# Optimization experiments

Measured on AMD Instinct MI355X. Metric: run time of the kernel, lower is better.

The kernel has to match this reference:

```python
import jax, jax.numpy as jnp
import numpy as np

DT_NS = 8.0
ALPHA, BETA, GAMMA, RISE_W = 0.7, 0.2, 0.1, 0.05
DECAY_TAUS = jnp.array([40.0, 300.0, 230.0, 2.4], dtype=jnp.float32)
RISE_TAUS = jnp.array([5.0, 20.0, 10.0, 2.0], dtype=jnp.float32)
TAIL = 195  # tail window: [peak+5, peak+200)


def setup_inputs() -> dict:
    key = jax.random.key(0)
    k1, k2, k3, k4 = jax.random.split(key, 4)
    B, S, C = 32768, 1024, 4
    return {
        "logits": jax.random.normal(k1, (B, C), dtype=jnp.float32),
        "labels": jax.random.randint(k2, (B,), 0, C, dtype=jnp.int64),
        "waveforms": jax.random.uniform(k3, (B, S), dtype=jnp.float32),
        "amplitudes": jax.random.uniform(k4, (B,), dtype=jnp.float32),
    }


def _masked_mean(vals, valid):
    w = valid.astype(vals.dtype)
    n = jnp.sum(w)
    return jnp.where(n > 0, jnp.sum(vals * w) / jnp.maximum(n, 1.0), 0.0)


def _decay_time_loss(waveforms, pred_cls):
    B, S = waveforms.shape
    peak = jnp.argmax(waveforms, axis=1)                      # (B,)
    valid = peak < S - 20
    # fixed-size tail window starting at peak+5, masked past end of record
    idx = peak[:, None] + 5 + jnp.arange(TAIL)[None, :]       # (B, TAIL)
    in_range = idx < S
    tail = jnp.take_along_axis(waveforms, jnp.minimum(idx, S - 1), axis=1)
    pos = in_range & (tail > 0)                               # positive-sample mask
    w = pos.astype(jnp.float32)
    n_pos = jnp.sum(w, axis=1)
    valid &= n_pos >= 5
    t = (jnp.arange(TAIL, dtype=jnp.float32) * DT_NS)[None, :]
    log_tail = jnp.log(jnp.where(pos, tail, 1.0) + 1e-8)
    n_safe = jnp.maximum(n_pos, 1.0)
    t_mean = jnp.sum(w * t, axis=1) / n_safe
    y_mean = jnp.sum(w * log_tail, axis=1) / n_safe
    dt_c = t - t_mean[:, None]
    num = jnp.sum(w * dt_c * (log_tail - y_mean[:, None]), axis=1)
    den = jnp.sum(w * dt_c * dt_c, axis=1)
    valid &= den > 0
    slope = num / jnp.maximum(den, 1e-30)
    fitted_tau = -1.0 / (slope + 1e-8)
    tau_loss = (fitted_tau - DECAY_TAUS[pred_cls]) ** 2
    return _masked_mean(tau_loss, valid)


def _energy_conservation_loss(waveforms, amplitudes):
    charge = jnp.sum(jnp.maximum(waveforms, 0.0), axis=1)
    ratio = charge / (amplitudes + 1e-8)
    return jnp.var(ratio, ddof=1)  # torch.var default is unbiased


def _rise_time_loss(waveforms, pred_cls):
    B, S = waveforms.shape
    peak = jnp.argmax(waveforms, axis=1)
    amp = jnp.take_along_axis(waveforms, peak[:, None], axis=1)[:, 0]
    valid = peak >= 10
    edge = jnp.arange(S)[None, :] < peak[:, None]             # rising edge mask
    ab10 = edge & (waveforms >= 0.1 * amp[:, None])
    ab90 = edge & (waveforms >= 0.9 * amp[:, None])
    valid &= jnp.any(ab10, axis=1) & jnp.any(ab90, axis=1)
    idx10 = jnp.argmax(ab10, axis=1).astype(jnp.float32)      # first crossing
    idx90 = jnp.argmax(ab90, axis=1).astype(jnp.float32)
    rise = (idx90 - idx10) * DT_NS
    exp_rise = RISE_TAUS[pred_cls]
    rt_loss = jnp.abs(rise - exp_rise) / exp_rise
    return _masked_mean(rt_loss, valid)


def reference(logits, labels, waveforms, amplitudes):
    logp = jax.nn.log_softmax(logits, axis=-1)
    ce = -jnp.mean(jnp.take_along_axis(logp, labels[:, None], axis=1)[:, 0])
    pred_cls = jnp.argmax(logits, axis=1)
    decay = _decay_time_loss(waveforms, pred_cls)
    energy = _energy_conservation_loss(waveforms, amplitudes)
    rise = _rise_time_loss(waveforms, pred_cls)
    total = ALPHA * ce + BETA * decay + GAMMA * energy + RISE_W * rise
    return total, ce, decay, energy, rise
```

## Files before the change

### kernel.cpp

```cpp
#include <hip/hip_runtime.h>
#include <cmath>

#define BROWS 32768
#define SLEN  1024
#define TAILW 195
#define NB1   2048
#define NB2   128

__device__ __constant__ float c_decay_taus[4] = {40.0f, 300.0f, 230.0f, 2.4f};
__device__ __constant__ float c_rise_taus[4]  = {5.0f, 20.0f, 10.0f, 2.0f};

struct alignas(16) RowStat {
    unsigned nSk;
    unsigned Skk;
    float    csum;
    unsigned pki;
    double   Sy;
    double   Sky;
};

extern "C" __global__ __launch_bounds__(256, 8)
void physics_rows(const float* __restrict__ wave, RowStat* __restrict__ stats)
{
    const int lane  = threadIdx.x & 63;
    const int wid   = threadIdx.x >> 6;
    const int gwave = blockIdx.x * 4 + wid;
    const int nwaves = NB1 * 4;
    const int lane4 = lane * 4;
    const float4* base = reinterpret_cast<const float4*>(wave);

    int row = gwave;
    const float4* p0 = base + (size_t)row * (SLEN / 4) + lane;
    float4 c0 = p0[0], c1 = p0[64], c2 = p0[128], c3 = p0[192];

    #pragma unroll
    for (int it = 0; it < 4; ++it) {
        const int nrow = row + nwaves;
        float4 n0, n1, n2, n3;
        if (it < 3) {
            const float4* pn = base + (size_t)nrow * (SLEN / 4) + lane;
            n0 = pn[0]; n1 = pn[64]; n2 = pn[128]; n3 = pn[192];
        }

        float vals[16] = {c0.x,c0.y,c0.z,c0.w, c1.x,c1.y,c1.z,c1.w,
                          c2.x,c2.y,c2.z,c2.w, c3.x,c3.y,c3.z,c3.w};

        float m0 = fmaxf(fmaxf(vals[0],  vals[1]),  vals[2]);
        float m1 = fmaxf(fmaxf(vals[3],  vals[4]),  vals[5]);
        float m2 = fmaxf(fmaxf(vals[6],  vals[7]),  vals[8]);
        float m3 = fmaxf(fmaxf(vals[9],  vals[10]), vals[11]);
        float m4 = fmaxf(fmaxf(vals[12], vals[13]), fmaxf(vals[14], vals[15]));
        float bm = fmaxf(fmaxf(fmaxf(m0, m1), m2), fmaxf(m3, m4));

        float s0 = 0.f, s1 = 0.f, s2 = 0.f, s3 = 0.f;
        #pragma unroll
        for (int k = 0; k < 16; k += 4) {
            s0 += fmaxf(vals[k],     0.0f);
            s1 += fmaxf(vals[k + 1], 0.0f);
            s2 += fmaxf(vals[k + 2], 0.0f);
            s3 += fmaxf(vals[k + 3], 0.0f);
        }
        float csum = (s0 + s1) + (s2 + s3);

        #pragma unroll
        for (int off = 1; off < 64; off <<= 1) {
            bm   = fmaxf(bm, __shfl_xor(bm, off, 64));
            csum += __shfl_xor(csum, off, 64);
        }
        const float amp = bm;

        int peak = SLEN;
        #pragma unroll
        for (int q = 0; q < 4; ++q) {
            bool found = false;
            #pragma unroll
            for (int r = 0; r < 4; ++r) {
                const unsigned long long b = __ballot(vals[q * 4 + r] == amp);
                if (b) {
                    peak = min(peak, q * 256 + 4 * (__ffsll(b) - 1) + r);
                    found = true;
                }
            }
            if (found) break;
        }
        peak = __builtin_amdgcn_readfirstlane(peak);
        const bool do_decay = (peak < SLEN - 20);
        const int  pm5 = peak + 5;

        const float t10 = 0.1f * amp, t90 = 0.9f * amp;
        int i10 = SLEN, i90 = SLEN;
        #pragma unroll
        for (int q = 0; q < 4; ++q) {
            #pragma unroll
            for (int r = 0; r < 4; ++r) {
                const int jb = q * 256 + r;
                const int d  = peak - jb;
                if (d > 0) {
                    const int lc = min(64, (d + 3) >> 2);
                    const unsigned long long lm =
                        (lc >= 64) ? ~0ull : ((1ull << lc) - 1ull);
                    const float w = vals[q * 4 + r];
                    const unsigned long long b10 = __ballot(w >= t10) & lm;
                    const unsigned long long b90 = __ballot(w >= t90) & lm;
                    if (b10) i10 = min(i10, jb + 4 * (__ffsll(b10) - 1));
                    if (b90) i90 = min(i90, jb + 4 * (__ffsll(b90) - 1));
                }
            }
        }

        unsigned nSk_p = 0, Skk = 0;
        double Sy = 0.0, Sky = 0.0;
        if (do_decay) {
            #pragma unroll
            for (int q = 0; q < 4; ++q) {
                if (q * 256 + 255 >= pm5 && q * 256 <= pm5 + (TAILW - 1)) {
                    #pragma unroll
                    for (int r = 0; r < 4; ++r) {
                        const int kk = q * 256 + lane4 + r - pm5;
                        const float w = vals[q * 4 + r];
                        if ((unsigned)kk < (unsigned)TAILW && w > 0.0f) {
                            const float y = __logf(w + 1e-8f);
                            nSk_p += 1u + ((unsigned)kk << 8);
                            Skk   += (unsigned)(kk * kk);
                            Sy  += (double)y;
                            Sky += (double)kk * (double)y;
                        }
                    }
                }
            }
        }

        #pragma unroll
        for (int off = 1; off < 64; off <<= 1) {
            nSk_p += __shfl_xor(nSk_p, off, 64);
            Skk   += __shfl_xor(Skk,   off, 64);
            Sy    += __shfl_xor(Sy,    off, 64);
            Sky   += __shfl_xor(Sky,   off, 64);
        }

        if (lane == 0) {
            RowStat st;
            st.nSk  = (nSk_p & 0xFFu) | ((nSk_p >> 8) << 16);
            st.Skk  = Skk;
            st.csum = csum;
            st.pki  = ((unsigned)peak << 22) | ((unsigned)i10 << 11) | (unsigned)i90;
            st.Sy   = Sy;
            st.Sky  = Sky;
            stats[row] = st;
        }

        if (it < 3) { c0 = n0; c1 = n1; c2 = n2; c3 = n3; row = nrow; }
    }
}

extern "C" __global__ __launch_bounds__(256)
void physics_rowfin(const RowStat* __restrict__ stats,
                    const float* __restrict__ logits,
                    const int* __restrict__ labels,
                    const float* __restrict__ amps,
                    double* __restrict__ partials)
{
    const int r    = blockIdx.x * 256 + threadIdx.x;
    const int lane = threadIdx.x & 63;
    const int wid  = threadIdx.x >> 6;

    const RowStat st = stats[r];
    const unsigned n_u  = st.nSk & 0xFFFFu;
    const unsigned Sk_u = st.nSk >> 16;
    const int peak = (int)(st.pki >> 22);
    const int i10  = (int)((st.pki >> 11) & 0x7FFu);
    const int i90  = (int)(st.pki & 0x7FFu);

    const float4 l4 = reinterpret_cast<const float4*>(logits)[r];
    float lg[4] = {l4.x, l4.y, l4.z, l4.w};
    int pred = 0; float pbest = lg[0];
    #pragma unroll
    for (int c = 1; c < 4; ++c) if (lg[c] > pbest) { pbest = lg[c]; pred = c; }
    const float m = fmaxf(fmaxf(lg[0], lg[1]), fmaxf(lg[2], lg[3]));
    const float sexp = expf(lg[0] - m) + expf(lg[1] - m)
                     + expf(lg[2] - m) + expf(lg[3] - m);
    const float lse = m + logf(sexp);
    const double v0 = (double)(lse - lg[labels[r]]);

    double v1 = 0.0, v2 = 0.0;
    if (peak < SLEN - 20 && n_u >= 5u) {
        const double dn  = (double)n_u;
        const double dSk = (double)Sk_u;
        const double num = st.Sky - dSk * st.Sy / dn;
        const double den = 8.0 * ((double)st.Skk - dSk * dSk / dn);
        if (den > 0.0) {
            const double slope = num / fmax(den, 1e-30);
            const double tau   = -1.0 / (slope + 1e-8);
            const double d     = tau - (double)c_decay_taus[pred];
            v1 = d * d; v2 = 1.0;
        }
    }
    double v3 = 0.0, v4 = 0.0;
    if (peak >= 10 && i10 < SLEN && i90 < SLEN) {
        const float rise = (float)(i90 - i10) * 8.0f;
        const float er   = c_rise_taus[pred];
        v3 = (double)(fabsf(rise - er) / er); v4 = 1.0;
    }
    const double ratio = (double)st.csum / ((double)amps[r] + 1e-8);

    double v[7] = {v0, v1, v2, v3, v4, ratio, ratio * ratio};
    #pragma unroll
    for (int i = 0; i < 7; ++i) {
        #pragma unroll
        for (int off = 1; off < 64; off <<= 1)
            v[i] += __shfl_xor(v[i], off, 64);
    }
    __shared__ double sm[4][7];
    if (lane == 0) {
        #pragma unroll
        for (int i = 0; i < 7; ++i) sm[wid][i] = v[i];
    }
    __syncthreads();
    if (threadIdx.x < 7) {
        const int i = threadIdx.x;
        partials[(size_t)blockIdx.x * 7 + i] = sm[0][i] + sm[1][i] + sm[2][i] + sm[3][i];
    }
}

extern "C" __global__ void physics_finalize(const double* __restrict__ partials,
                                            float* __restrict__ out)
{
    const int t = threadIdx.x;
    double loc[7];
    #pragma unroll
    for (int i = 0; i < 7; ++i)
        loc[i] = partials[(size_t)t * 7 + i] + partials[(size_t)(t + 64) * 7 + i];
    #pragma unroll
    for (int i = 0; i < 7; ++i) {
        #pragma unroll
        for (int off = 1; off < 64; off <<= 1)
            loc[i] += __shfl_xor(loc[i], off, 64);
    }
    if (t == 0) {
        const double Bn = (double)BROWS;
        const double ce    = loc[0] / Bn;
        const double decay = (loc[2] > 0.0) ? loc[1] / fmax(loc[2], 1.0) : 0.0;
        const double rise  = (loc[4] > 0.0) ? loc[3] / fmax(loc[4], 1.0) : 0.0;
        const double var   = (loc[6] - loc[5] * loc[5] / Bn) / (Bn - 1.0);
        const double total = 0.7 * ce + 0.2 * decay + 0.1 * var + 0.05 * rise;
        out[0] = (float)total; out[1] = (float)ce; out[2] = (float)decay;
        out[3] = (float)var;   out[4] = (float)rise;
    }
}

extern "C" void kernel_launch(void* const* d_in, const int* in_sizes, int n_in,
                              void* d_out, int out_size, void* d_ws, size_t ws_size,
                              hipStream_t stream) {
    const float* logits = (const float*)d_in[0];
    const int*   labels = (const int*)d_in[1];
    const float* wave   = (const float*)d_in[2];
    const float* amps   = (const float*)d_in[3];

    RowStat* stats    = (RowStat*)d_ws;
    double*  partials = (double*)((char*)d_ws + (size_t)BROWS * sizeof(RowStat));

    physics_rows<<<NB1, 256, 0, stream>>>(wave, stats);
    physics_rowfin<<<NB2, 256, 0, stream>>>(stats, logits, labels, amps, partials);
    physics_finalize<<<1, 64, 0, stream>>>(partials, (float*)d_out);
}
```

Baseline: 46.13 us.

## Fuse row stats, per-row finalize and global reduction into one kernel

Merges the three kernels into a single kernel. Per-row statistics stay in shared memory and are finalized in-block rather than written to a workspace and re-read. A global atomic counter lets the last block reduce the per-block partials and write the outputs. This removes two kernel launches and the stats round trip through memory. In exchange it adds a memset, atomics and a serial tail in one block.

```diff
diff --git a/kernel.cpp b/kernel.cpp
--- a/kernel.cpp
+++ b/kernel.cpp
@@ -5,39 +5,42 @@
 #define SLEN  1024
 #define TAILW 195
 #define NB1   2048
-#define NB2   128
+#define NWAVES (NB1 * 4)
+#define RPW   4
+#define PART_STRIDE 2048
 
 __device__ __constant__ float c_decay_taus[4] = {40.0f, 300.0f, 230.0f, 2.4f};
 __device__ __constant__ float c_rise_taus[4]  = {5.0f, 20.0f, 10.0f, 2.0f};
 
-struct alignas(16) RowStat {
-    unsigned nSk;
-    unsigned Skk;
-    float    csum;
-    unsigned pki;
-    double   Sy;
-    double   Sky;
-};
-
 extern "C" __global__ __launch_bounds__(256, 8)
-void physics_rows(const float* __restrict__ wave, RowStat* __restrict__ stats)
+void physics_fused(const float* __restrict__ wave,
+                   const float* __restrict__ logits,
+                   const int*   __restrict__ labels,
+                   const float* __restrict__ amps,
+                   double* __restrict__ partials,
+                   unsigned* __restrict__ counter,
+                   float* __restrict__ out)
 {
     const int lane  = threadIdx.x & 63;
     const int wid   = threadIdx.x >> 6;
     const int gwave = blockIdx.x * 4 + wid;
-    const int nwaves = NB1 * 4;
     const int lane4 = lane * 4;
     const float4* base = reinterpret_cast<const float4*>(wave);
+
+    __shared__ unsigned su[4][RPW][4];
+    __shared__ double   sd[4][RPW][2];
+    __shared__ double   smp[4][7];
+    __shared__ int      s_last;
 
     int row = gwave;
     const float4* p0 = base + (size_t)row * (SLEN / 4) + lane;
     float4 c0 = p0[0], c1 = p0[64], c2 = p0[128], c3 = p0[192];
 
     #pragma unroll
-    for (int it = 0; it < 4; ++it) {
-        const int nrow = row + nwaves;
+    for (int it = 0; it < RPW; ++it) {
+        const int nrow = row + NWAVES;
         float4 n0, n1, n2, n3;
-        if (it < 3) {
+        if (it < RPW - 1) {
             const float4* pn = base + (size_t)nrow * (SLEN / 4) + lane;
             n0 = pn[0]; n1 = pn[64]; n2 = pn[128]; n3 = pn[192];
         }
@@ -139,109 +142,123 @@
         }
 
         if (lane == 0) {
-            RowStat st;
-            st.nSk  = (nSk_p & 0xFFu) | ((nSk_p >> 8) << 16);
-            st.Skk  = Skk;
-            st.csum = csum;
-            st.pki  = ((unsigned)peak << 22) | ((unsigned)i10 << 11) | (unsigned)i90;
-            st.Sy   = Sy;
-            st.Sky  = Sky;
-            stats[row] = st;
-        }
-
-        if (it < 3) { c0 = n0; c1 = n1; c2 = n2; c3 = n3; row = nrow; }
-    }
-}
-
-extern "C" __global__ __launch_bounds__(256)
-void physics_rowfin(const RowStat* __restrict__ stats,
-                    const float* __restrict__ logits,
-                    const int* __restrict__ labels,
-                    const float* __restrict__ amps,
-                    double* __restrict__ partials)
-{
-    const int r    = blockIdx.x * 256 + threadIdx.x;
-    const int lane = threadIdx.x & 63;
-    const int wid  = threadIdx.x >> 6;
-
-    const RowStat st = stats[r];
-    const unsigned n_u  = st.nSk & 0xFFFFu;
-    const unsigned Sk_u = st.nSk >> 16;
-    const int peak = (int)(st.pki >> 22);
-    const int i10  = (int)((st.pki >> 11) & 0x7FFu);
-    const int i90  = (int)(st.pki & 0x7FFu);
-
-    const float4 l4 = reinterpret_cast<const float4*>(logits)[r];
-    float lg[4] = {l4.x, l4.y, l4.z, l4.w};
-    int pred = 0; float pbest = lg[0];
-    #pragma unroll
-    for (int c = 1; c < 4; ++c) if (lg[c] > pbest) { pbest = lg[c]; pred = c; }
-    const float m = fmaxf(fmaxf(lg[0], lg[1]), fmaxf(lg[2], lg[3]));
-    const float sexp = expf(lg[0] - m) + expf(lg[1] - m)
-                     + expf(lg[2] - m) + expf(lg[3] - m);
-    const float lse = m + logf(sexp);
-    const double v0 = (double)(lse - lg[labels[r]]);
-
-    double v1 = 0.0, v2 = 0.0;
-    if (peak < SLEN - 20 && n_u >= 5u) {
-        const double dn  = (double)n_u;
-        const double dSk = (double)Sk_u;
-        const double num = st.Sky - dSk * st.Sy / dn;
-        const double den = 8.0 * ((double)st.Skk - dSk * dSk / dn);
-        if (den > 0.0) {
-            const double slope = num / fmax(den, 1e-30);
-            const double tau   = -1.0 / (slope + 1e-8);
-            const double d     = tau - (double)c_decay_taus[pred];
-            v1 = d * d; v2 = 1.0;
-        }
-    }
-    double v3 = 0.0, v4 = 0.0;
-    if (peak >= 10 && i10 < SLEN && i90 < SLEN) {
-        const float rise = (float)(i90 - i10) * 8.0f;
-        const float er   = c_rise_taus[pred];
-        v3 = (double)(fabsf(rise - er) / er); v4 = 1.0;
-    }
-    const double ratio = (double)st.csum / ((double)amps[r] + 1e-8);
-
-    double v[7] = {v0, v1, v2, v3, v4, ratio, ratio * ratio};
-    #pragma unroll
-    for (int i = 0; i < 7; ++i) {
-        #pragma unroll
-        for (int off = 1; off < 64; off <<= 1)
-            v[i] += __shfl_xor(v[i], off, 64);
-    }
-    __shared__ double sm[4][7];
+            su[wid][it][0] = nSk_p;
+            su[wid][it][1] = Skk;
+            su[wid][it][2] = __float_as_uint(csum);
+            su[wid][it][3] = ((unsigned)peak << 22) | ((unsigned)i10 << 11) | (unsigned)i90;
+            sd[wid][it][0] = Sy;
+            sd[wid][it][1] = Sky;
+        }
+
+        if (it < RPW - 1) { c0 = n0; c1 = n1; c2 = n2; c3 = n3; row = nrow; }
+    }
+
+    double v0 = 0, v1 = 0, v2 = 0, v3 = 0, v4 = 0, v5 = 0, v6 = 0;
+    if (lane < RPW) {
+        const int r = gwave + lane * NWAVES;
+        const unsigned nSk = su[wid][lane][0];
+        const unsigned Skk = su[wid][lane][1];
+        const float   csum = __uint_as_float(su[wid][lane][2]);
+        const unsigned pki = su[wid][lane][3];
+        const double  Sy   = sd[wid][lane][0];
+        const double  Sky  = sd[wid][lane][1];
+        const unsigned n_u  = nSk & 0xFFu;
+        const unsigned Sk_u = nSk >> 8;
+        const int peak = (int)(pki >> 22);
+        const int i10  = (int)((pki >> 11) & 0x7FFu);
+        const int i90  = (int)(pki & 0x7FFu);
+
+        const float4 l4 = reinterpret_cast<const float4*>(logits)[r];
+        float lg[4] = {l4.x, l4.y, l4.z, l4.w};
+        int pred = 0; float pbest = lg[0];
+        #pragma unroll
+        for (int c = 1; c < 4; ++c) if (lg[c] > pbest) { pbest = lg[c]; pred = c; }
+        const float m = fmaxf(fmaxf(lg[0], lg[1]), fmaxf(lg[2], lg[3]));
+        const float sexp = expf(lg[0] - m) + expf(lg[1] - m)
+                         + expf(lg[2] - m) + expf(lg[3] - m);
+        const float lse = m + logf(sexp);
+        v0 = (double)(lse - lg[labels[r]]);
+
+        if (peak < SLEN - 20 && n_u >= 5u) {
+            const double dn  = (double)n_u;
+            const double dSk = (double)Sk_u;
+            const double num = Sky - dSk * Sy / dn;
+            const double den = 8.0 * ((double)Skk - dSk * dSk / dn);
+            if (den > 0.0) {
+                const double slope = num / fmax(den, 1e-30);
+                const double tau   = -1.0 / (slope + 1e-8);
+                const double d     = tau - (double)c_decay_taus[pred];
+                v1 = d * d; v2 = 1.0;
+            }
+        }
+        if (peak >= 10 && i10 < SLEN && i90 < SLEN) {
+            const float rise = (float)(i90 - i10) * 8.0f;
+            const float er   = c_rise_taus[pred];
+            v3 = (double)(fabsf(rise - er) / er); v4 = 1.0;
+        }
+        v5 = (double)csum / ((double)amps[r] + 1e-8);
+        v6 = v5 * v5;
+    }
+    #pragma unroll
+    for (int off = 1; off <= 2; off <<= 1) {
+        v0 += __shfl_xor(v0, off, 64);
+        v1 += __shfl_xor(v1, off, 64);
+        v2 += __shfl_xor(v2, off, 64);
+        v3 += __shfl_xor(v3, off, 64);
+        v4 += __shfl_xor(v4, off, 64);
+        v5 += __shfl_xor(v5, off, 64);
+        v6 += __shfl_xor(v6, off, 64);
+    }
     if (lane == 0) {
-        #pragma unroll
-        for (int i = 0; i < 7; ++i) sm[wid][i] = v[i];
+        smp[wid][0] = v0; smp[wid][1] = v1; smp[wid][2] = v2; smp[wid][3] = v3;
+        smp[wid][4] = v4; smp[wid][5] = v5; smp[wid][6] = v6;
     }
     __syncthreads();
     if (threadIdx.x < 7) {
         const int i = threadIdx.x;
-        partials[(size_t)blockIdx.x * 7 + i] = sm[0][i] + sm[1][i] + sm[2][i] + sm[3][i];
-    }
-}
-
-extern "C" __global__ void physics_finalize(const double* __restrict__ partials,
-                                            float* __restrict__ out)
-{
-    const int t = threadIdx.x;
-    double loc[7];
-    #pragma unroll
-    for (int i = 0; i < 7; ++i)
-        loc[i] = partials[(size_t)t * 7 + i] + partials[(size_t)(t + 64) * 7 + i];
+        const double t = smp[0][i] + smp[1][i] + smp[2][i] + smp[3][i];
+        __hip_atomic_store(&partials[(size_t)i * PART_STRIDE + blockIdx.x], t,
+                           __ATOMIC_RELAXED, __HIP_MEMORY_SCOPE_AGENT);
+    }
+    __syncthreads();
+    if (threadIdx.x == 0) {
+        const unsigned prev = __hip_atomic_fetch_add(counter, 1u,
+                                  __ATOMIC_ACQ_REL, __HIP_MEMORY_SCOPE_AGENT);
+        s_last = (prev == NB1 - 1) ? 1 : 0;
+    }
+    __syncthreads();
+    if (!s_last) return;
+
+    double loc[7] = {0, 0, 0, 0, 0, 0, 0};
+    #pragma unroll
+    for (int k = 0; k < NB1 / 256; ++k) {
+        const int b = k * 256 + threadIdx.x;
+        #pragma unroll
+        for (int i = 0; i < 7; ++i)
+            loc[i] += __hip_atomic_load(&partials[(size_t)i * PART_STRIDE + b],
+                                        __ATOMIC_RELAXED, __HIP_MEMORY_SCOPE_AGENT);
+    }
     #pragma unroll
     for (int i = 0; i < 7; ++i) {
         #pragma unroll
         for (int off = 1; off < 64; off <<= 1)
             loc[i] += __shfl_xor(loc[i], off, 64);
     }
-    if (t == 0) {
+    if (lane == 0) {
+        #pragma unroll
+        for (int i = 0; i < 7; ++i) smp[wid][i] = loc[i];
+    }
+    __syncthreads();
+    if (threadIdx.x == 0) {
+        double t[7];
+        #pragma unroll
+        for (int i = 0; i < 7; ++i)
+            t[i] = smp[0][i] + smp[1][i] + smp[2][i] + smp[3][i];
         const double Bn = (double)BROWS;
-        const double ce    = loc[0] / Bn;
-        const double decay = (loc[2] > 0.0) ? loc[1] / fmax(loc[2], 1.0) : 0.0;
-        const double rise  = (loc[4] > 0.0) ? loc[3] / fmax(loc[4], 1.0) : 0.0;
-        const double var   = (loc[6] - loc[5] * loc[5] / Bn) / (Bn - 1.0);
+        const double ce    = t[0] / Bn;
+        const double decay = (t[2] > 0.0) ? t[1] / fmax(t[2], 1.0) : 0.0;
+        const double rise  = (t[4] > 0.0) ? t[3] / fmax(t[4], 1.0) : 0.0;
+        const double var   = (t[6] - t[5] * t[5] / Bn) / (Bn - 1.0);
         const double total = 0.7 * ce + 0.2 * decay + 0.1 * var + 0.05 * rise;
         out[0] = (float)total; out[1] = (float)ce; out[2] = (float)decay;
         out[3] = (float)var;   out[4] = (float)rise;
@@ -256,10 +273,10 @@
     const float* wave   = (const float*)d_in[2];
     const float* amps   = (const float*)d_in[3];
 
-    RowStat* stats    = (RowStat*)d_ws;
-    double*  partials = (double*)((char*)d_ws + (size_t)BROWS * sizeof(RowStat));
-
-    physics_rows<<<NB1, 256, 0, stream>>>(wave, stats);
-    physics_rowfin<<<NB2, 256, 0, stream>>>(stats, logits, labels, amps, partials);
-    physics_finalize<<<1, 64, 0, stream>>>(partials, (float*)d_out);
+    double*   partials = (double*)d_ws;
+    unsigned* counter  = (unsigned*)((char*)d_ws + 7 * PART_STRIDE * sizeof(double));
+
+    hipMemsetAsync(counter, 0, sizeof(unsigned), stream);
+    physics_fused<<<NB1, 256, 0, stream>>>(wave, logits, labels, amps,
+                                           partials, counter, (float*)d_out);
 }
```

After: 77.89 us. 1.69x slower.

## Drop software row pipelining and fold finalize into last-block reduction

Applied to the files above, without the earlier changes.

The row kernel now launches one wavefront per row (8192 blocks) instead of a persistent grid that prefetched the next row, so latency hiding relies on occupancy rather than explicit double-buffering. The separate finalize kernel is removed: each rowfin block publishes its partials, increments an atomic counter, and the last block performs the final reduction and writes outputs. This removes a kernel launch but adds a memset node and atomic synchronization.

```diff
diff --git a/kernel.cpp b/kernel.cpp
--- a/kernel.cpp
+++ b/kernel.cpp
@@ -4,8 +4,9 @@
 #define BROWS 32768
 #define SLEN  1024
 #define TAILW 195
-#define NB1   2048
+#define NB1   8192
 #define NB2   128
+#define PSTRIDE 128
 
 __device__ __constant__ float c_decay_taus[4] = {40.0f, 300.0f, 230.0f, 2.4f};
 __device__ __constant__ float c_rise_taus[4]  = {5.0f, 20.0f, 10.0f, 2.0f};
@@ -22,134 +23,117 @@
 extern "C" __global__ __launch_bounds__(256, 8)
 void physics_rows(const float* __restrict__ wave, RowStat* __restrict__ stats)
 {
-    const int lane  = threadIdx.x & 63;
-    const int wid   = threadIdx.x >> 6;
-    const int gwave = blockIdx.x * 4 + wid;
-    const int nwaves = NB1 * 4;
+    const int lane = threadIdx.x & 63;
+    const int row  = (blockIdx.x * 256 + threadIdx.x) >> 6;
     const int lane4 = lane * 4;
-    const float4* base = reinterpret_cast<const float4*>(wave);
-
-    int row = gwave;
-    const float4* p0 = base + (size_t)row * (SLEN / 4) + lane;
-    float4 c0 = p0[0], c1 = p0[64], c2 = p0[128], c3 = p0[192];
-
-    #pragma unroll
-    for (int it = 0; it < 4; ++it) {
-        const int nrow = row + nwaves;
-        float4 n0, n1, n2, n3;
-        if (it < 3) {
-            const float4* pn = base + (size_t)nrow * (SLEN / 4) + lane;
-            n0 = pn[0]; n1 = pn[64]; n2 = pn[128]; n3 = pn[192];
-        }
-
-        float vals[16] = {c0.x,c0.y,c0.z,c0.w, c1.x,c1.y,c1.z,c1.w,
-                          c2.x,c2.y,c2.z,c2.w, c3.x,c3.y,c3.z,c3.w};
-
-        float m0 = fmaxf(fmaxf(vals[0],  vals[1]),  vals[2]);
-        float m1 = fmaxf(fmaxf(vals[3],  vals[4]),  vals[5]);
-        float m2 = fmaxf(fmaxf(vals[6],  vals[7]),  vals[8]);
-        float m3 = fmaxf(fmaxf(vals[9],  vals[10]), vals[11]);
-        float m4 = fmaxf(fmaxf(vals[12], vals[13]), fmaxf(vals[14], vals[15]));
-        float bm = fmaxf(fmaxf(fmaxf(m0, m1), m2), fmaxf(m3, m4));
-
-        float s0 = 0.f, s1 = 0.f, s2 = 0.f, s3 = 0.f;
-        #pragma unroll
-        for (int k = 0; k < 16; k += 4) {
-            s0 += fmaxf(vals[k],     0.0f);
-            s1 += fmaxf(vals[k + 1], 0.0f);
-            s2 += fmaxf(vals[k + 2], 0.0f);
-            s3 += fmaxf(vals[k + 3], 0.0f);
-        }
-        float csum = (s0 + s1) + (s2 + s3);
-
-        #pragma unroll
-        for (int off = 1; off < 64; off <<= 1) {
-            bm   = fmaxf(bm, __shfl_xor(bm, off, 64));
-            csum += __shfl_xor(csum, off, 64);
-        }
-        const float amp = bm;
-
-        int peak = SLEN;
+    const float4* p = reinterpret_cast<const float4*>(wave) + (size_t)row * (SLEN / 4) + lane;
+
+    const float4 c0 = p[0], c1 = p[64], c2 = p[128], c3 = p[192];
+    float vals[16] = {c0.x,c0.y,c0.z,c0.w, c1.x,c1.y,c1.z,c1.w,
+                      c2.x,c2.y,c2.z,c2.w, c3.x,c3.y,c3.z,c3.w};
+
+    float m0 = fmaxf(fmaxf(vals[0],  vals[1]),  vals[2]);
+    float m1 = fmaxf(fmaxf(vals[3],  vals[4]),  vals[5]);
+    float m2 = fmaxf(fmaxf(vals[6],  vals[7]),  vals[8]);
+    float m3 = fmaxf(fmaxf(vals[9],  vals[10]), vals[11]);
+    float m4 = fmaxf(fmaxf(vals[12], vals[13]), fmaxf(vals[14], vals[15]));
+    float bm = fmaxf(fmaxf(fmaxf(m0, m1), m2), fmaxf(m3, m4));
+
+    float s0 = 0.f, s1 = 0.f, s2 = 0.f, s3 = 0.f;
+    #pragma unroll
+    for (int k = 0; k < 16; k += 4) {
+        s0 += fmaxf(vals[k],     0.0f);
+        s1 += fmaxf(vals[k + 1], 0.0f);
+        s2 += fmaxf(vals[k + 2], 0.0f);
+        s3 += fmaxf(vals[k + 3], 0.0f);
+    }
+    float csum = (s0 + s1) + (s2 + s3);
+
+    #pragma unroll
+    for (int off = 1; off < 64; off <<= 1) {
+        bm   = fmaxf(bm, __shfl_xor(bm, off, 64));
+        csum += __shfl_xor(csum, off, 64);
+    }
+    const float amp = bm;
+
+    int peak = SLEN;
+    #pragma unroll
+    for (int q = 0; q < 4; ++q) {
+        bool found = false;
+        #pragma unroll
+        for (int r = 0; r < 4; ++r) {
+            const unsigned long long b = __ballot(vals[q * 4 + r] == amp);
+            if (b) {
+                peak = min(peak, q * 256 + 4 * (__ffsll(b) - 1) + r);
+                found = true;
+            }
+        }
+        if (found) break;
+    }
+    peak = __builtin_amdgcn_readfirstlane(peak);
+    const bool do_decay = (peak < SLEN - 20);
+    const int  pm5 = peak + 5;
+
+    const float t10 = 0.1f * amp, t90 = 0.9f * amp;
+    int i10 = SLEN, i90 = SLEN;
+    #pragma unroll
+    for (int q = 0; q < 4; ++q) {
+        #pragma unroll
+        for (int r = 0; r < 4; ++r) {
+            const int jb = q * 256 + r;
+            const int d  = peak - jb;
+            if (d > 0) {
+                const int lc = min(64, (d + 3) >> 2);
+                const unsigned long long lm =
+                    (lc >= 64) ? ~0ull : ((1ull << lc) - 1ull);
+                const float w = vals[q * 4 + r];
+                const unsigned long long b10 = __ballot(w >= t10) & lm;
+                const unsigned long long b90 = __ballot(w >= t90) & lm;
+                if (b10) i10 = min(i10, jb + 4 * (__ffsll(b10) - 1));
+                if (b90) i90 = min(i90, jb + 4 * (__ffsll(b90) - 1));
+            }
+        }
+    }
+
+    unsigned nSk_p = 0, Skk = 0;
+    double Sy = 0.0, Sky = 0.0;
+    if (do_decay) {
         #pragma unroll
         for (int q = 0; q < 4; ++q) {
-            bool found = false;
-            #pragma unroll
-            for (int r = 0; r < 4; ++r) {
-                const unsigned long long b = __ballot(vals[q * 4 + r] == amp);
-                if (b) {
-                    peak = min(peak, q * 256 + 4 * (__ffsll(b) - 1) + r);
-                    found = true;
-                }
-            }
-            if (found) break;
-        }
-        peak = __builtin_amdgcn_readfirstlane(peak);
-        const bool do_decay = (peak < SLEN - 20);
-        const int  pm5 = peak + 5;
-
-        const float t10 = 0.1f * amp, t90 = 0.9f * amp;
-        int i10 = SLEN, i90 = SLEN;
-        #pragma unroll
-        for (int q = 0; q < 4; ++q) {
-            #pragma unroll
-            for (int r = 0; r < 4; ++r) {
-                const int jb = q * 256 + r;
-                const int d  = peak - jb;
-                if (d > 0) {
-                    const int lc = min(64, (d + 3) >> 2);
-                    const unsigned long long lm =
-                        (lc >= 64) ? ~0ull : ((1ull << lc) - 1ull);
+            if (q * 256 + 255 >= pm5 && q * 256 <= pm5 + (TAILW - 1)) {
+                #pragma unroll
+                for (int r = 0; r < 4; ++r) {
+                    const int kk = q * 256 + lane4 + r - pm5;
                     const float w = vals[q * 4 + r];
-                    const unsigned long long b10 = __ballot(w >= t10) & lm;
-                    const unsigned long long b90 = __ballot(w >= t90) & lm;
-                    if (b10) i10 = min(i10, jb + 4 * (__ffsll(b10) - 1));
-                    if (b90) i90 = min(i90, jb + 4 * (__ffsll(b90) - 1));
-                }
-            }
-        }
-
-        unsigned nSk_p = 0, Skk = 0;
-        double Sy = 0.0, Sky = 0.0;
-        if (do_decay) {
-            #pragma unroll
-            for (int q = 0; q < 4; ++q) {
-                if (q * 256 + 255 >= pm5 && q * 256 <= pm5 + (TAILW - 1)) {
-                    #pragma unroll
-                    for (int r = 0; r < 4; ++r) {
-                        const int kk = q * 256 + lane4 + r - pm5;
-                        const float w = vals[q * 4 + r];
-                        if ((unsigned)kk < (unsigned)TAILW && w > 0.0f) {
-                            const float y = __logf(w + 1e-8f);
-                            nSk_p += 1u + ((unsigned)kk << 8);
-                            Skk   += (unsigned)(kk * kk);
-                            Sy  += (double)y;
-                            Sky += (double)kk * (double)y;
-                        }
+                    if ((unsigned)kk < (unsigned)TAILW && w > 0.0f) {
+                        const float y = __logf(w + 1e-8f);
+                        nSk_p += 1u + ((unsigned)kk << 8);
+                        Skk   += (unsigned)(kk * kk);
+                        Sy  += (double)y;
+                        Sky += (double)kk * (double)y;
                     }
                 }
             }
         }
-
-        #pragma unroll
-        for (int off = 1; off < 64; off <<= 1) {
-            nSk_p += __shfl_xor(nSk_p, off, 64);
-            Skk   += __shfl_xor(Skk,   off, 64);
-            Sy    += __shfl_xor(Sy,    off, 64);
-            Sky   += __shfl_xor(Sky,   off, 64);
-        }
-
-        if (lane == 0) {
-            RowStat st;
-            st.nSk  = (nSk_p & 0xFFu) | ((nSk_p >> 8) << 16);
-            st.Skk  = Skk;
-            st.csum = csum;
-            st.pki  = ((unsigned)peak << 22) | ((unsigned)i10 << 11) | (unsigned)i90;
-            st.Sy   = Sy;
-            st.Sky  = Sky;
-            stats[row] = st;
-        }
-
-        if (it < 3) { c0 = n0; c1 = n1; c2 = n2; c3 = n3; row = nrow; }
+    }
+
+    #pragma unroll
+    for (int off = 1; off < 64; off <<= 1) {
+        nSk_p += __shfl_xor(nSk_p, off, 64);
+        Skk   += __shfl_xor(Skk,   off, 64);
+        Sy    += __shfl_xor(Sy,    off, 64);
+        Sky   += __shfl_xor(Sky,   off, 64);
+    }
+
+    if (lane == 0) {
+        RowStat st;
+        st.nSk  = (nSk_p & 0xFFu) | ((nSk_p >> 8) << 16);
+        st.Skk  = Skk;
+        st.csum = csum;
+        st.pki  = ((unsigned)peak << 22) | ((unsigned)i10 << 11) | (unsigned)i90;
+        st.Sy   = Sy;
+        st.Sky  = Sky;
+        stats[row] = st;
     }
 }
 
@@ -158,11 +142,16 @@
                     const float* __restrict__ logits,
                     const int* __restrict__ labels,
                     const float* __restrict__ amps,
-                    double* __restrict__ partials)
+                    double* __restrict__ partials,
+                    unsigned* __restrict__ counter,
+                    float* __restrict__ out)
 {
     const int r    = blockIdx.x * 256 + threadIdx.x;
     const int lane = threadIdx.x & 63;
     const int wid  = threadIdx.x >> 6;
+
+    __shared__ double sm[4][7];
+    __shared__ int s_last;
 
     const RowStat st = stats[r];
     const unsigned n_u  = st.nSk & 0xFFFFu;
@@ -210,7 +199,6 @@
         for (int off = 1; off < 64; off <<= 1)
             v[i] += __shfl_xor(v[i], off, 64);
     }
-    __shared__ double sm[4][7];
     if (lane == 0) {
         #pragma unroll
         for (int i = 0; i < 7; ++i) sm[wid][i] = v[i];
@@ -218,30 +206,47 @@
     __syncthreads();
     if (threadIdx.x < 7) {
         const int i = threadIdx.x;
-        partials[(size_t)blockIdx.x * 7 + i] = sm[0][i] + sm[1][i] + sm[2][i] + sm[3][i];
-    }
-}
-
-extern "C" __global__ void physics_finalize(const double* __restrict__ partials,
-                                            float* __restrict__ out)
-{
-    const int t = threadIdx.x;
-    double loc[7];
-    #pragma unroll
-    for (int i = 0; i < 7; ++i)
-        loc[i] = partials[(size_t)t * 7 + i] + partials[(size_t)(t + 64) * 7 + i];
+        const double t = sm[0][i] + sm[1][i] + sm[2][i] + sm[3][i];
+        __hip_atomic_store(&partials[(size_t)i * PSTRIDE + blockIdx.x], t,
+                           __ATOMIC_RELAXED, __HIP_MEMORY_SCOPE_AGENT);
+    }
+    __syncthreads();
+    if (threadIdx.x == 0) {
+        const unsigned prev = __hip_atomic_fetch_add(counter, 1u,
+                                  __ATOMIC_ACQ_REL, __HIP_MEMORY_SCOPE_AGENT);
+        s_last = (prev == NB2 - 1) ? 1 : 0;
+    }
+    __syncthreads();
+    if (!s_last) return;
+
+    double loc[7] = {0, 0, 0, 0, 0, 0, 0};
+    if (threadIdx.x < PSTRIDE) {
+        #pragma unroll
+        for (int i = 0; i < 7; ++i)
+            loc[i] = __hip_atomic_load(&partials[(size_t)i * PSTRIDE + threadIdx.x],
+                                       __ATOMIC_RELAXED, __HIP_MEMORY_SCOPE_AGENT);
+    }
     #pragma unroll
     for (int i = 0; i < 7; ++i) {
         #pragma unroll
         for (int off = 1; off < 64; off <<= 1)
             loc[i] += __shfl_xor(loc[i], off, 64);
     }
-    if (t == 0) {
+    __syncthreads();
+    if (lane == 0 && wid < 2) {
+        #pragma unroll
+        for (int i = 0; i < 7; ++i) sm[wid][i] = loc[i];
+    }
+    __syncthreads();
+    if (threadIdx.x == 0) {
+        double t[7];
+        #pragma unroll
+        for (int i = 0; i < 7; ++i) t[i] = sm[0][i] + sm[1][i];
         const double Bn = (double)BROWS;
-        const double ce    = loc[0] / Bn;
-        const double decay = (loc[2] > 0.0) ? loc[1] / fmax(loc[2], 1.0) : 0.0;
-        const double rise  = (loc[4] > 0.0) ? loc[3] / fmax(loc[4], 1.0) : 0.0;
-        const double var   = (loc[6] - loc[5] * loc[5] / Bn) / (Bn - 1.0);
+        const double ce    = t[0] / Bn;
+        const double decay = (t[2] > 0.0) ? t[1] / fmax(t[2], 1.0) : 0.0;
+        const double rise  = (t[4] > 0.0) ? t[3] / fmax(t[4], 1.0) : 0.0;
+        const double var   = (t[6] - t[5] * t[5] / Bn) / (Bn - 1.0);
         const double total = 0.7 * ce + 0.2 * decay + 0.1 * var + 0.05 * rise;
         out[0] = (float)total; out[1] = (float)ce; out[2] = (float)decay;
         out[3] = (float)var;   out[4] = (float)rise;
@@ -256,10 +261,12 @@
     const float* wave   = (const float*)d_in[2];
     const float* amps   = (const float*)d_in[3];
 
-    RowStat* stats    = (RowStat*)d_ws;
-    double*  partials = (double*)((char*)d_ws + (size_t)BROWS * sizeof(RowStat));
-
+    RowStat*  stats    = (RowStat*)d_ws;
+    double*   partials = (double*)((char*)d_ws + (size_t)BROWS * sizeof(RowStat));
+    unsigned* counter  = (unsigned*)((char*)partials + 7 * PSTRIDE * sizeof(double));
+
+    hipMemsetAsync(counter, 0, sizeof(unsigned), stream);
     physics_rows<<<NB1, 256, 0, stream>>>(wave, stats);
-    physics_rowfin<<<NB2, 256, 0, stream>>>(stats, logits, labels, amps, partials);
-    physics_finalize<<<1, 64, 0, stream>>>(partials, (float*)d_out);
+    physics_rowfin<<<NB2, 256, 0, stream>>>(stats, logits, labels, amps,
+                                            partials, counter, (float*)d_out);
 }
```

Result: faster. 45.16 us (-2.1%).
